# Kernel tuning notes

Measured on AMD Instinct MI355X. Metric: run time of the kernel, lower is better.

## Reference

```python
import jax, jax.numpy as jnp
import numpy as np

B, S, HID = 1, 4096, 3584
NH, NKV, HD = 16, 8, 256
Q_SIZE, KV_SIZE = NH * HD, NKV * HD
SCALE = 256.0 ** -0.5          # query_pre_attn_scalar ** -0.5
SOFTCAP = 50.0                 # attn_logit_softcapping
WINDOW = 2048 - 1              # effective sliding window (sliding_window - 1)
THETA = 10000.0                # rope_theta
NEG = -1e30


def setup_inputs() -> dict:
    key = jax.random.key(0)
    k1, k2, k3 = jax.random.split(key, 3)
    hidden_states = jax.random.normal(k1, (B, S, HID), dtype=jnp.float32)
    position_ids = jnp.arange(S, dtype=jnp.int64).reshape(1, S)
    w_qkv = jax.random.normal(k2, (Q_SIZE + 2 * KV_SIZE, HID), dtype=jnp.float32) * 0.02
    w_o = jax.random.normal(k3, (HID, Q_SIZE), dtype=jnp.float32) * 0.02
    return {"position_ids": position_ids, "hidden_states": hidden_states,
            "w_qkv": w_qkv, "w_o": w_o}


def _rope_neox(x, pos):
    # x: [B, S, n_heads, HD]; pos: [B, S]
    half = HD // 2
    inv_freq = 1.0 / (THETA ** (jnp.arange(half, dtype=jnp.float32) * 2.0 / HD))
    ang = pos.astype(jnp.float32)[..., None] * inv_freq          # [B, S, half]
    cos = jnp.cos(ang)[:, :, None, :]                            # [B, S, 1, half]
    sin = jnp.sin(ang)[:, :, None, :]
    x1, x2 = x[..., :half], x[..., half:]
    return jnp.concatenate([x1 * cos - x2 * sin, x2 * cos + x1 * sin], axis=-1)


def reference(position_ids, hidden_states, w_qkv, w_o):
    # QKV projection (no bias)
    qkv = hidden_states @ w_qkv.T                                # [B, S, Q+2KV]
    q = qkv[..., :Q_SIZE].reshape(B, S, NH, HD)
    k = qkv[..., Q_SIZE:Q_SIZE + KV_SIZE].reshape(B, S, NKV, HD)
    v = qkv[..., Q_SIZE + KV_SIZE:].reshape(B, S, NKV, HD)

    # Neox-style RoPE over full head_dim
    q = _rope_neox(q, position_ids)
    k = _rope_neox(k, position_ids)

    # GQA: expand kv heads to query heads
    rep = NH // NKV
    k = jnp.repeat(k, rep, axis=2)                               # [B, S, NH, HD]
    v = jnp.repeat(v, rep, axis=2)

    # Scaled scores with tanh logit softcapping
    scores = jnp.einsum('bqhd,bkhd->bhqk', q, k) * SCALE
    scores = SOFTCAP * jnp.tanh(scores / SOFTCAP)

    # Causal + sliding-window mask: j <= i and i - j <= WINDOW
    i = jnp.arange(S)[:, None]
    j = jnp.arange(S)[None, :]
    mask = (j <= i) & (i - j <= WINDOW)                          # [S, S]
    scores = jnp.where(mask[None, None, :, :], scores, NEG)

    probs = jax.nn.softmax(scores, axis=-1)
    attn = jnp.einsum('bhqk,bkhd->bqhd', probs, v).reshape(B, S, Q_SIZE)

    # Output projection (no bias)
    return attn @ w_o.T                                          # [B, S, HID]
```

## Files before the change

kernel.cpp:

```cpp
#include <hip/hip_runtime.h>
#include <cstdint>
#include <cstddef>

#define S_LEN 4096
#define HID   3584
#define NH    16
#define NKV   8
#define HD    256
#define QSZ   (NH*HD)
#define KVSZ  (NKV*HD)
#define QKV_N (QSZ + 2*KVSZ)
#define WINDOW 2047

typedef unsigned short u16;
typedef __bf16 bf16x8 __attribute__((ext_vector_type(8)));
typedef u16    u16x8  __attribute__((ext_vector_type(8)));
typedef u16    u16x4  __attribute__((ext_vector_type(4)));
typedef float  f32x4  __attribute__((ext_vector_type(4)));

__device__ inline float bf2f(u16 u) {
    union { unsigned u; float f; } v; v.u = ((unsigned)u) << 16; return v.f;
}
__device__ inline u16 f2bf(float f) {
    union { float f; unsigned u; } v; v.f = f;
    return (u16)((v.u + 0x7FFF + ((v.u >> 16) & 1)) >> 16);
}
__device__ inline float fast_tanh(float x) {
    x = fminf(fmaxf(x, -20.f), 20.f);
    float e = __expf(2.f * x);
    return 1.f - 2.f / (e + 1.f);
}

__global__ __launch_bounds__(256)
void cast_f32_bf16(const float* __restrict__ src, u16* __restrict__ dst, int n4) {
    int i = blockIdx.x * blockDim.x + threadIdx.x;
    if (i >= n4) return;
    float4 v = ((const float4*)src)[i];
    u16x4 o;
    o[0] = f2bf(v.x); o[1] = f2bf(v.y); o[2] = f2bf(v.z); o[3] = f2bf(v.w);
    ((u16x4*)dst)[i] = o;
}

template<int BF16OUT>
__global__ __launch_bounds__(256)
void gemm_bt(const u16* __restrict__ A, const u16* __restrict__ B,
             void* __restrict__ Cv, int M, int N, int K) {
    __shared__ u16 lA[128 * 32];
    __shared__ u16 lB[128 * 32];
    const int tid  = threadIdx.x;
    const int lane = tid & 63, wave = tid >> 6;
    const int quad = lane >> 4, l16 = lane & 15;
    const int m0 = blockIdx.y * 128, n0 = blockIdx.x * 128;
    const int wm = (wave & 1) * 64, wn = (wave >> 1) * 64;

    f32x4 zero = {0.f, 0.f, 0.f, 0.f};
    f32x4 acc[4][4];
#pragma unroll
    for (int i = 0; i < 4; ++i)
#pragma unroll
        for (int j = 0; j < 4; ++j) acc[i][j] = zero;

    const int c0 = tid, c1 = tid + 256;
    const int r0 = c0 >> 2, cc0 = (c0 & 3) * 8;
    const int r1 = c1 >> 2, cc1 = (c1 & 3) * 8;
    const u16* A0 = A + (size_t)(m0 + r0) * K + cc0;
    const u16* A1 = A + (size_t)(m0 + r1) * K + cc1;
    const u16* B0 = B + (size_t)(n0 + r0) * K + cc0;
    const u16* B1 = B + (size_t)(n0 + r1) * K + cc1;

    u16x8 ra0 = *(const u16x8*)A0;
    u16x8 ra1 = *(const u16x8*)A1;
    u16x8 rb0 = *(const u16x8*)B0;
    u16x8 rb1 = *(const u16x8*)B1;

    for (int k0 = 0; k0 < K; k0 += 32) {
        __syncthreads();
        *(u16x8*)(&lA[c0 * 8]) = ra0;
        *(u16x8*)(&lA[c1 * 8]) = ra1;
        *(u16x8*)(&lB[c0 * 8]) = rb0;
        *(u16x8*)(&lB[c1 * 8]) = rb1;
        __syncthreads();
        int kn = k0 + 32;
        if (kn < K) {
            ra0 = *(const u16x8*)(A0 + kn);
            ra1 = *(const u16x8*)(A1 + kn);
            rb0 = *(const u16x8*)(B0 + kn);
            rb1 = *(const u16x8*)(B1 + kn);
        }
        bf16x8 af[4], bfr[4];
#pragma unroll
        for (int mt = 0; mt < 4; ++mt)
            af[mt] = *(const bf16x8*)(&lA[(wm + mt * 16 + l16) * 32 + quad * 8]);
#pragma unroll
        for (int nt = 0; nt < 4; ++nt)
            bfr[nt] = *(const bf16x8*)(&lB[(wn + nt * 16 + l16) * 32 + quad * 8]);
#pragma unroll
        for (int mt = 0; mt < 4; ++mt)
#pragma unroll
            for (int nt = 0; nt < 4; ++nt)
                acc[mt][nt] = __builtin_amdgcn_mfma_f32_16x16x32_bf16(
                    af[mt], bfr[nt], acc[mt][nt], 0, 0, 0);
    }

#pragma unroll
    for (int mt = 0; mt < 4; ++mt)
#pragma unroll
        for (int nt = 0; nt < 4; ++nt)
#pragma unroll
            for (int r = 0; r < 4; ++r) {
                int row = m0 + wm + mt * 16 + quad * 4 + r;
                int col = n0 + wn + nt * 16 + l16;
                float v = acc[mt][nt][r];
                if (BF16OUT) ((u16*)Cv)[(size_t)row * N + col] = f2bf(v);
                else         ((float*)Cv)[(size_t)row * N + col] = v;
            }
}

__global__ __launch_bounds__(256)
void rope_split(const u16* __restrict__ qkv, u16* __restrict__ Qb,
                u16* __restrict__ Kb, u16* __restrict__ Vb) {
    const int s = blockIdx.x;
    const int t = threadIdx.x;
    const float pos = (float)s;
    const u16* row = qkv + (size_t)s * QKV_N;

    for (int p = t; p < 2048; p += 256) {
        int h = p >> 7, d = p & 127;
        float inv = __expf(-(float)d * 0.0719557841560639f);
        float ang = pos * inv, sn, cs;
        sincosf(ang, &sn, &cs);
        float x1 = bf2f(row[h * HD + d]);
        float x2 = bf2f(row[h * HD + d + 128]);
        size_t base = ((size_t)h * S_LEN + s) * HD;
        Qb[base + d]       = f2bf((x1 * cs - x2 * sn) * 0.0625f);
        Qb[base + d + 128] = f2bf((x2 * cs + x1 * sn) * 0.0625f);
    }
    for (int p = t; p < 1024; p += 256) {
        int h = p >> 7, d = p & 127;
        float inv = __expf(-(float)d * 0.0719557841560639f);
        float ang = pos * inv, sn, cs;
        sincosf(ang, &sn, &cs);
        float x1 = bf2f(row[QSZ + h * HD + d]);
        float x2 = bf2f(row[QSZ + h * HD + d + 128]);
        size_t base = ((size_t)h * S_LEN + s) * HD;
        Kb[base + d]       = f2bf(x1 * cs - x2 * sn);
        Kb[base + d + 128] = f2bf(x2 * cs + x1 * sn);
    }
    for (int e = t; e < 2048; e += 256) {
        int h = e >> 8, d = e & 255;
        Vb[((size_t)h * S_LEN + s) * HD + d] = row[QSZ + KVSZ + e];
    }
}

__global__ __launch_bounds__(256)
void attn_fused(const u16* __restrict__ Qb, const u16* __restrict__ Kb,
                const u16* __restrict__ Vb, u16* __restrict__ O) {
    const int h  = blockIdx.y;
    const int qt = blockIdx.x;
    const int hkv = h >> 1;
    const int qbase = qt * 64;
    const int tid = threadIdx.x, wave = tid >> 6, lane = tid & 63;
    const int quad = lane >> 4, l16 = lane & 15;

    __shared__ u16 lK[32 * 264];
    __shared__ u16 lV[256 * 40];
    __shared__ u16 lP[4][16 * 40];

    const int qrow = qbase + wave * 16 + l16;
    bf16x8 qf[8];
    {
        const u16* qp = Qb + ((size_t)h * S_LEN + qrow) * HD + quad * 8;
#pragma unroll
        for (int f = 0; f < 8; ++f) qf[f] = *(const bf16x8*)(qp + f * 32);
    }

    f32x4 zero = {0.f, 0.f, 0.f, 0.f};
    f32x4 o[16];
#pragma unroll
    for (int i = 0; i < 16; ++i) o[i] = zero;
    float m_r[4], l_r[4];
#pragma unroll
    for (int r = 0; r < 4; ++r) { m_r[r] = -1e4f; l_r[r] = 0.f; }

    const int t0 = max(0, qbase - WINDOW) >> 5;
    const int t1 = (qbase + 63) >> 5;
    const u16* Kh = Kb + (size_t)hkv * S_LEN * HD;
    const u16* Vh = Vb + (size_t)hkv * S_LEN * HD;

    for (int kt = t0; kt <= t1; ++kt) {
        const int kb = kt * 32;
        __syncthreads();
#pragma unroll
        for (int it = 0; it < 4; ++it) {
            int c = tid + it * 256;
            int krow = c >> 5;
            int col = (c & 31) * 8;
            *(u16x8*)(&lK[krow * 264 + col]) =
                *(const u16x8*)(Kh + (size_t)(kb + krow) * HD + col);
        }
        {
            int key = tid & 31;
            int db0 = (tid >> 5) * 8;
#pragma unroll
            for (int it = 0; it < 4; ++it) {
                int dbase = db0 + it * 64;
                u16x8 v = *(const u16x8*)(Vh + (size_t)(kb + key) * HD + dbase);
#pragma unroll
                for (int j = 0; j < 8; ++j) lV[(dbase + j) * 40 + key] = v[j];
            }
        }
        __syncthreads();

        f32x4 sc[2];
#pragma unroll
        for (int ct = 0; ct < 2; ++ct) {
            f32x4 a = zero;
#pragma unroll
            for (int f = 0; f < 8; ++f) {
                bf16x8 kf = *(const bf16x8*)(&lK[(ct * 16 + l16) * 264 + f * 32 + quad * 8]);
                a = __builtin_amdgcn_mfma_f32_16x16x32_bf16(qf[f], kf, a, 0, 0, 0);
            }
            sc[ct] = a;
        }

        float p0[4], p1[4], rowmax[4];
#pragma unroll
        for (int r = 0; r < 4; ++r) {
            const int gi = qbase + wave * 16 + quad * 4 + r;
            float x0 = 50.f * fast_tanh(sc[0][r] * 0.02f);
            float x1 = 50.f * fast_tanh(sc[1][r] * 0.02f);
            int gj0 = kb + l16, gj1 = kb + 16 + l16;
            bool ok0 = (gj0 <= gi) && (gi - gj0 <= WINDOW);
            bool ok1 = (gj1 <= gi) && (gi - gj1 <= WINDOW);
            p0[r] = ok0 ? x0 : -1e30f;
            p1[r] = ok1 ? x1 : -1e30f;
            rowmax[r] = fmaxf(p0[r], p1[r]);
        }
#pragma unroll
        for (int m = 1; m < 16; m <<= 1)
#pragma unroll
            for (int r = 0; r < 4; ++r)
                rowmax[r] = fmaxf(rowmax[r], __shfl_xor(rowmax[r], m, 64));

        float al[4], rs[4];
#pragma unroll
        for (int r = 0; r < 4; ++r) {
            float mn = fmaxf(m_r[r], rowmax[r]);
            al[r] = __expf(m_r[r] - mn);
            m_r[r] = mn;
            float e0 = __expf(p0[r] - mn);
            float e1 = __expf(p1[r] - mn);
            p0[r] = e0; p1[r] = e1;
            rs[r] = e0 + e1;
        }
#pragma unroll
        for (int m = 1; m < 16; m <<= 1)
#pragma unroll
            for (int r = 0; r < 4; ++r)
                rs[r] += __shfl_xor(rs[r], m, 64);

        u16* pw = &lP[wave][0];
#pragma unroll
        for (int r = 0; r < 4; ++r) {
            l_r[r] = l_r[r] * al[r] + rs[r];
            pw[(quad * 4 + r) * 40 + l16]      = f2bf(p0[r]);
            pw[(quad * 4 + r) * 40 + 16 + l16] = f2bf(p1[r]);
        }
#pragma unroll
        for (int dt = 0; dt < 16; ++dt)
#pragma unroll
            for (int r = 0; r < 4; ++r) o[dt][r] *= al[r];

        asm volatile("s_waitcnt lgkmcnt(0)" ::: "memory");
        bf16x8 pf = *(const bf16x8*)(&pw[l16 * 40 + quad * 8]);
#pragma unroll
        for (int dt = 0; dt < 16; ++dt) {
            bf16x8 vf = *(const bf16x8*)(&lV[(dt * 16 + l16) * 40 + quad * 8]);
            o[dt] = __builtin_amdgcn_mfma_f32_16x16x32_bf16(pf, vf, o[dt], 0, 0, 0);
        }
    }

    float inv_l[4];
#pragma unroll
    for (int r = 0; r < 4; ++r) inv_l[r] = 1.f / l_r[r];
#pragma unroll
    for (int dt = 0; dt < 16; ++dt)
#pragma unroll
        for (int r = 0; r < 4; ++r) {
            int grow = qbase + wave * 16 + quad * 4 + r;
            int gcol = h * HD + dt * 16 + l16;
            O[(size_t)grow * QSZ + gcol] = f2bf(o[dt][r] * inv_l[r]);
        }
}

extern "C" void kernel_launch(void* const* d_in, const int* in_sizes, int n_in,
                              void* d_out, int out_size, void* d_ws, size_t ws_size,
                              hipStream_t stream) {
    const float* hidden = (const float*)d_in[1];
    const float* w_qkv  = (const float*)d_in[2];
    const float* w_o    = (const float*)d_in[3];
    float* out = (float*)d_out;

    char* ws = (char*)d_ws;
    size_t off = 0;
    auto alloc = [&](size_t bytes) {
        void* p = ws + off; off += (bytes + 255) & ~(size_t)255; return p;
    };
    u16* Xb    = (u16*)alloc((size_t)S_LEN * HID   * 2);
    u16* Wqkvb = (u16*)alloc((size_t)QKV_N * HID   * 2);
    u16* QKVb  = (u16*)alloc((size_t)S_LEN * QKV_N * 2);
    u16* Qb    = (u16*)alloc((size_t)NH  * S_LEN * HD * 2);
    u16* Kb    = (u16*)alloc((size_t)NKV * S_LEN * HD * 2);
    u16* Vb    = (u16*)alloc((size_t)NKV * S_LEN * HD * 2);
    u16* attn  = QKVb;
    u16* Wob   = Xb;

    const int n1 = S_LEN * HID / 4;
    const int n2 = QKV_N * HID / 4;

    cast_f32_bf16<<<dim3((n1 + 255) / 256), dim3(256), 0, stream>>>(hidden, Xb, n1);
    cast_f32_bf16<<<dim3((n2 + 255) / 256), dim3(256), 0, stream>>>(w_qkv, Wqkvb, n2);
    gemm_bt<1><<<dim3(QKV_N / 128, S_LEN / 128), dim3(256), 0, stream>>>(
        Xb, Wqkvb, (void*)QKVb, S_LEN, QKV_N, HID);
    rope_split<<<dim3(S_LEN), dim3(256), 0, stream>>>(QKVb, Qb, Kb, Vb);
    cast_f32_bf16<<<dim3((n1 + 255) / 256), dim3(256), 0, stream>>>(w_o, Wob, n1);
    attn_fused<<<dim3(S_LEN / 64, NH), dim3(256), 0, stream>>>(Qb, Kb, Vb, attn);
    gemm_bt<0><<<dim3(HID / 128, S_LEN / 128), dim3(256), 0, stream>>>(
        attn, Wob, (void*)out, S_LEN, HID, QSZ);
}
```

Measured before the change: 1.196 ms.

## Pre-transpose V and load K/V tiles to LDS via direct global_load_lds

V is transposed once in a new kernel into a d-major layout, so the attention kernel can pull K and V tiles straight into swizzled LDS with global_load_lds. This replaces register-staged copies and the scalar per-element V transpose scatter inside the hot loop. The attention loop also skips per-wave work on key tiles fully outside that wave's causal/sliding window. It adds a lazy max-rescale that only rescales the accumulators when the row max grows by more than 8. The costs are an extra kernel launch and full pass over V, and the lazy rescale slightly changes the numerics of the softmax.

```diff
diff --git a/kernel.cpp b/kernel.cpp
--- a/kernel.cpp
+++ b/kernel.cpp
@@ -29,6 +29,13 @@
     x = fminf(fmaxf(x, -20.f), 20.f);
     float e = __expf(2.f * x);
     return 1.f - 2.f / (e + 1.f);
+}
+
+typedef const __attribute__((address_space(1))) unsigned GU32;
+typedef __attribute__((address_space(3))) unsigned LU32;
+__device__ inline void gll16(const void* g, const void* l) {
+    __builtin_amdgcn_global_load_lds((GU32*)(size_t)g,
+                                     (LU32*)(unsigned)(size_t)l, 16, 0, 0);
 }
 
 __global__ __launch_bounds__(256)
@@ -118,7 +125,7 @@
 
 __global__ __launch_bounds__(256)
 void rope_split(const u16* __restrict__ qkv, u16* __restrict__ Qb,
-                u16* __restrict__ Kb, u16* __restrict__ Vb) {
+                u16* __restrict__ Kb) {
     const int s = blockIdx.x;
     const int t = threadIdx.x;
     const float pos = (float)s;
@@ -146,15 +153,35 @@
         Kb[base + d]       = f2bf(x1 * cs - x2 * sn);
         Kb[base + d + 128] = f2bf(x2 * cs + x1 * sn);
     }
-    for (int e = t; e < 2048; e += 256) {
-        int h = e >> 8, d = e & 255;
-        Vb[((size_t)h * S_LEN + s) * HD + d] = row[QSZ + KVSZ + e];
+}
+
+__global__ __launch_bounds__(256)
+void transpose_v(const u16* __restrict__ qkv, u16* __restrict__ Vt) {
+    const int h = blockIdx.x, s0 = blockIdx.y * 64;
+    const int tid = threadIdx.x;
+    __shared__ u16 t[64 * 258];
+    const u16* src = qkv + QSZ + KVSZ + (size_t)h * HD;
+#pragma unroll
+    for (int it = 0; it < 8; ++it) {
+        int idx = it * 256 + tid;
+        int sr = idx >> 5, c8 = (idx & 31) << 3;
+        u16x8 v = *(const u16x8*)(src + (size_t)(s0 + sr) * QKV_N + c8);
+#pragma unroll
+        for (int j = 0; j < 8; ++j) t[sr * 258 + c8 + j] = v[j];
+    }
+    __syncthreads();
+    const int lane = tid & 63, wave = tid >> 6;
+    u16* dst = Vt + (size_t)h * HD * S_LEN + s0 + lane;
+#pragma unroll
+    for (int it = 0; it < 64; ++it) {
+        int d = it * 4 + wave;
+        dst[(size_t)d * S_LEN] = t[lane * 258 + d];
     }
 }
 
 __global__ __launch_bounds__(256)
 void attn_fused(const u16* __restrict__ Qb, const u16* __restrict__ Kb,
-                const u16* __restrict__ Vb, u16* __restrict__ O) {
+                const u16* __restrict__ Vt, u16* __restrict__ O) {
     const int h  = blockIdx.y;
     const int qt = blockIdx.x;
     const int hkv = h >> 1;
@@ -162,11 +189,12 @@
     const int tid = threadIdx.x, wave = tid >> 6, lane = tid & 63;
     const int quad = lane >> 4, l16 = lane & 15;
 
-    __shared__ u16 lK[32 * 264];
-    __shared__ u16 lV[256 * 40];
-    __shared__ u16 lP[4][16 * 40];
-
-    const int qrow = qbase + wave * 16 + l16;
+    __shared__ __align__(16) u16 lK[32 * 256];
+    __shared__ __align__(16) u16 lV[32 * 256];
+    __shared__ __align__(16) u16 lP[4][16 * 40];
+
+    const int qw = qbase + wave * 16;
+    const int qrow = qw + l16;
     bf16x8 qf[8];
     {
         const u16* qp = Qb + ((size_t)h * S_LEN + qrow) * HD + quad * 8;
@@ -174,6 +202,22 @@
         for (int f = 0; f < 8; ++f) qf[f] = *(const bf16x8*)(qp + f * 32);
     }
 
+    int koff[4], voff[4];
+#pragma unroll
+    for (int i = 0; i < 4; ++i) {
+        int c = i * 256 + tid;
+        int row = c >> 5, j = c & 31;
+        koff[i] = row * 512 + ((j ^ (row & 7)) << 4);
+        int d = c >> 2;
+        int q = (c & 3) ^ ((d >> 1) & 3);
+        voff[i] = d * S_LEN * 2 + q * 16;
+    }
+    const char* Khb = (const char*)(Kb + (size_t)hkv * S_LEN * HD);
+    const char* Vhb = (const char*)(Vt + (size_t)hkv * HD * S_LEN);
+
+    const unsigned vrow = (unsigned)(l16 * 64)
+                        + ((unsigned)(quad ^ ((l16 >> 1) & 3)) << 4);
+
     f32x4 zero = {0.f, 0.f, 0.f, 0.f};
     f32x4 o[16];
 #pragma unroll
@@ -184,99 +228,110 @@
 
     const int t0 = max(0, qbase - WINDOW) >> 5;
     const int t1 = (qbase + 63) >> 5;
-    const u16* Kh = Kb + (size_t)hkv * S_LEN * HD;
-    const u16* Vh = Vb + (size_t)hkv * S_LEN * HD;
 
     for (int kt = t0; kt <= t1; ++kt) {
         const int kb = kt * 32;
         __syncthreads();
-#pragma unroll
-        for (int it = 0; it < 4; ++it) {
-            int c = tid + it * 256;
-            int krow = c >> 5;
-            int col = (c & 31) * 8;
-            *(u16x8*)(&lK[krow * 264 + col]) =
-                *(const u16x8*)(Kh + (size_t)(kb + krow) * HD + col);
+        {
+            const char* kp = Khb + ((size_t)kb << 9);
+            const char* vp = Vhb + ((size_t)kb << 1);
+#pragma unroll
+            for (int i = 0; i < 4; ++i) {
+                gll16(kp + koff[i], (const char*)lK + i * 4096 + wave * 1024);
+                gll16(vp + voff[i], (const char*)lV + i * 4096 + wave * 1024);
+            }
         }
-        {
-            int key = tid & 31;
-            int db0 = (tid >> 5) * 8;
-#pragma unroll
-            for (int it = 0; it < 4; ++it) {
-                int dbase = db0 + it * 64;
-                u16x8 v = *(const u16x8*)(Vh + (size_t)(kb + key) * HD + dbase);
-#pragma unroll
-                for (int j = 0; j < 8; ++j) lV[(dbase + j) * 40 + key] = v[j];
-            }
-        }
+        asm volatile("s_waitcnt vmcnt(0)" ::: "memory");
         __syncthreads();
 
-        f32x4 sc[2];
-#pragma unroll
-        for (int ct = 0; ct < 2; ++ct) {
-            f32x4 a = zero;
-#pragma unroll
-            for (int f = 0; f < 8; ++f) {
-                bf16x8 kf = *(const bf16x8*)(&lK[(ct * 16 + l16) * 264 + f * 32 + quad * 8]);
-                a = __builtin_amdgcn_mfma_f32_16x16x32_bf16(qf[f], kf, a, 0, 0, 0);
-            }
-            sc[ct] = a;
-        }
-
-        float p0[4], p1[4], rowmax[4];
-#pragma unroll
-        for (int r = 0; r < 4; ++r) {
-            const int gi = qbase + wave * 16 + quad * 4 + r;
-            float x0 = 50.f * fast_tanh(sc[0][r] * 0.02f);
-            float x1 = 50.f * fast_tanh(sc[1][r] * 0.02f);
-            int gj0 = kb + l16, gj1 = kb + 16 + l16;
-            bool ok0 = (gj0 <= gi) && (gi - gj0 <= WINDOW);
-            bool ok1 = (gj1 <= gi) && (gi - gj1 <= WINDOW);
-            p0[r] = ok0 ? x0 : -1e30f;
-            p1[r] = ok1 ? x1 : -1e30f;
-            rowmax[r] = fmaxf(p0[r], p1[r]);
-        }
-#pragma unroll
-        for (int m = 1; m < 16; m <<= 1)
-#pragma unroll
-            for (int r = 0; r < 4; ++r)
-                rowmax[r] = fmaxf(rowmax[r], __shfl_xor(rowmax[r], m, 64));
-
-        float al[4], rs[4];
-#pragma unroll
-        for (int r = 0; r < 4; ++r) {
-            float mn = fmaxf(m_r[r], rowmax[r]);
-            al[r] = __expf(m_r[r] - mn);
-            m_r[r] = mn;
-            float e0 = __expf(p0[r] - mn);
-            float e1 = __expf(p1[r] - mn);
-            p0[r] = e0; p1[r] = e1;
-            rs[r] = e0 + e1;
-        }
-#pragma unroll
-        for (int m = 1; m < 16; m <<= 1)
-#pragma unroll
-            for (int r = 0; r < 4; ++r)
-                rs[r] += __shfl_xor(rs[r], m, 64);
-
-        u16* pw = &lP[wave][0];
-#pragma unroll
-        for (int r = 0; r < 4; ++r) {
-            l_r[r] = l_r[r] * al[r] + rs[r];
-            pw[(quad * 4 + r) * 40 + l16]      = f2bf(p0[r]);
-            pw[(quad * 4 + r) * 40 + 16 + l16] = f2bf(p1[r]);
-        }
-#pragma unroll
-        for (int dt = 0; dt < 16; ++dt)
-#pragma unroll
-            for (int r = 0; r < 4; ++r) o[dt][r] *= al[r];
-
-        asm volatile("s_waitcnt lgkmcnt(0)" ::: "memory");
-        bf16x8 pf = *(const bf16x8*)(&pw[l16 * 40 + quad * 8]);
-#pragma unroll
-        for (int dt = 0; dt < 16; ++dt) {
-            bf16x8 vf = *(const bf16x8*)(&lV[(dt * 16 + l16) * 40 + quad * 8]);
-            o[dt] = __builtin_amdgcn_mfma_f32_16x16x32_bf16(pf, vf, o[dt], 0, 0, 0);
+        if ((kb <= qw + 15) && (kb + 31 >= qw - WINDOW)) {
+            f32x4 sc[2];
+#pragma unroll
+            for (int ct = 0; ct < 2; ++ct) {
+                f32x4 a = zero;
+                const char* kbase = (const char*)lK + (ct * 16 + l16) * 512;
+                const unsigned swz = (unsigned)((l16 & 7) << 4);
+#pragma unroll
+                for (int f = 0; f < 8; ++f) {
+                    bf16x8 kf = *(const bf16x8*)(
+                        kbase + (((unsigned)(f * 64 + quad * 16)) ^ swz));
+                    a = __builtin_amdgcn_mfma_f32_16x16x32_bf16(qf[f], kf, a, 0, 0, 0);
+                }
+                sc[ct] = a;
+            }
+
+            float p0[4], p1[4], rowmax[4];
+#pragma unroll
+            for (int r = 0; r < 4; ++r) {
+                const int gi = qw + quad * 4 + r;
+                float x0 = 50.f * fast_tanh(sc[0][r] * 0.02f);
+                float x1 = 50.f * fast_tanh(sc[1][r] * 0.02f);
+                int gj0 = kb + l16, gj1 = kb + 16 + l16;
+                bool ok0 = (gj0 <= gi) && (gi - gj0 <= WINDOW);
+                bool ok1 = (gj1 <= gi) && (gi - gj1 <= WINDOW);
+                p0[r] = ok0 ? x0 : -1e30f;
+                p1[r] = ok1 ? x1 : -1e30f;
+                rowmax[r] = fmaxf(p0[r], p1[r]);
+            }
+#pragma unroll
+            for (int m = 1; m < 16; m <<= 1)
+#pragma unroll
+                for (int r = 0; r < 4; ++r)
+                    rowmax[r] = fmaxf(rowmax[r], __shfl_xor(rowmax[r], m, 64));
+
+            float need = -1e30f;
+#pragma unroll
+            for (int r = 0; r < 4; ++r) need = fmaxf(need, rowmax[r] - m_r[r]);
+            const bool upd = __any(need > 8.f) != 0;
+            float al[4];
+            if (upd) {
+#pragma unroll
+                for (int r = 0; r < 4; ++r) {
+                    float mn = fmaxf(m_r[r], rowmax[r]);
+                    al[r] = __expf(m_r[r] - mn);
+                    m_r[r] = mn;
+                }
+            }
+
+            float rs[4];
+#pragma unroll
+            for (int r = 0; r < 4; ++r) {
+                p0[r] = __expf(p0[r] - m_r[r]);
+                p1[r] = __expf(p1[r] - m_r[r]);
+                rs[r] = p0[r] + p1[r];
+            }
+#pragma unroll
+            for (int m = 1; m < 16; m <<= 1)
+#pragma unroll
+                for (int r = 0; r < 4; ++r)
+                    rs[r] += __shfl_xor(rs[r], m, 64);
+
+            if (upd) {
+#pragma unroll
+                for (int dt = 0; dt < 16; ++dt)
+#pragma unroll
+                    for (int r = 0; r < 4; ++r) o[dt][r] *= al[r];
+#pragma unroll
+                for (int r = 0; r < 4; ++r) l_r[r] = l_r[r] * al[r] + rs[r];
+            } else {
+#pragma unroll
+                for (int r = 0; r < 4; ++r) l_r[r] += rs[r];
+            }
+
+            u16* pw = &lP[wave][0];
+#pragma unroll
+            for (int r = 0; r < 4; ++r) {
+                pw[(quad * 4 + r) * 40 + l16]      = f2bf(p0[r]);
+                pw[(quad * 4 + r) * 40 + 16 + l16] = f2bf(p1[r]);
+            }
+            asm volatile("s_waitcnt lgkmcnt(0)" ::: "memory");
+            bf16x8 pf = *(const bf16x8*)(&pw[l16 * 40 + quad * 8]);
+
+#pragma unroll
+            for (int dt = 0; dt < 16; ++dt) {
+                bf16x8 vf = *(const bf16x8*)((const char*)lV + dt * 1024 + vrow);
+                o[dt] = __builtin_amdgcn_mfma_f32_16x16x32_bf16(pf, vf, o[dt], 0, 0, 0);
+            }
         }
     }
 
@@ -311,7 +366,7 @@
     u16* QKVb  = (u16*)alloc((size_t)S_LEN * QKV_N * 2);
     u16* Qb    = (u16*)alloc((size_t)NH  * S_LEN * HD * 2);
     u16* Kb    = (u16*)alloc((size_t)NKV * S_LEN * HD * 2);
-    u16* Vb    = (u16*)alloc((size_t)NKV * S_LEN * HD * 2);
+    u16* Vt    = (u16*)alloc((size_t)NKV * S_LEN * HD * 2);
     u16* attn  = QKVb;
     u16* Wob   = Xb;
 
@@ -322,9 +377,10 @@
     cast_f32_bf16<<<dim3((n2 + 255) / 256), dim3(256), 0, stream>>>(w_qkv, Wqkvb, n2);
     gemm_bt<1><<<dim3(QKV_N / 128, S_LEN / 128), dim3(256), 0, stream>>>(
         Xb, Wqkvb, (void*)QKVb, S_LEN, QKV_N, HID);
-    rope_split<<<dim3(S_LEN), dim3(256), 0, stream>>>(QKVb, Qb, Kb, Vb);
+    rope_split<<<dim3(S_LEN), dim3(256), 0, stream>>>(QKVb, Qb, Kb);
+    transpose_v<<<dim3(NKV, S_LEN / 64), dim3(256), 0, stream>>>(QKVb, Vt);
     cast_f32_bf16<<<dim3((n1 + 255) / 256), dim3(256), 0, stream>>>(w_o, Wob, n1);
-    attn_fused<<<dim3(S_LEN / 64, NH), dim3(256), 0, stream>>>(Qb, Kb, Vb, attn);
+    attn_fused<<<dim3(S_LEN / 64, NH), dim3(256), 0, stream>>>(Qb, Kb, Vt, attn);
     gemm_bt<0><<<dim3(HID / 128, S_LEN / 128), dim3(256), 0, stream>>>(
         attn, Wob, (void*)out, S_LEN, HID, QSZ);
 }
```

Measured after the change: 1.510 ms. 1.26x slower.
